# Optimization experiments

Measured on AMD Instinct MI355X. Metric: run time of the kernel, lower is better.

## Reference

```python
import jax, jax.numpy as jnp
import numpy as np

K = 9  # ATSS top-k candidates per GT


def cxcywh_to_xyxy(b):
    cx, cy, w, h = b[..., 0], b[..., 1], b[..., 2], b[..., 3]
    return jnp.stack([cx - 0.5 * w, cy - 0.5 * h, cx + 0.5 * w, cy + 0.5 * h], axis=-1)


def elementwise_iou(a, b):
    # a, b: [..., 4] xyxy, broadcastable
    lt = jnp.maximum(a[..., :2], b[..., :2])
    rb = jnp.minimum(a[..., 2:], b[..., 2:])
    wh = jnp.clip(rb - lt, 0.0)
    inter = wh[..., 0] * wh[..., 1]
    area_a = (a[..., 2] - a[..., 0]) * (a[..., 3] - a[..., 1])
    area_b = (b[..., 2] - b[..., 0]) * (b[..., 3] - b[..., 1])
    return inter / (area_a + area_b - inter)


def setup_inputs() -> dict:
    key = jax.random.key(0)
    k1, k2 = jax.random.split(key)
    pred_boxes = jax.random.uniform(k1, (16, 30000, 4), dtype=jnp.float32)
    gt_boxes = jax.random.uniform(k2, (16, 64, 4), dtype=jnp.float32)
    return {"pred_boxes": pred_boxes, "gt_boxes": gt_boxes}


def reference(pred_boxes, gt_boxes):
    # pred_boxes: [B, N, 4] cxcywh; gt_boxes: [B, G, 4] cxcywh
    G = gt_boxes.shape[1]

    def per_image(pred, gt):
        # center-distance matrix [G, N] (the cdist in the original)
        diff = gt[:, None, :2] - pred[None, :, :2]
        dist = jnp.sqrt(jnp.sum(diff * diff, axis=-1))
        # k smallest distances per GT
        _, k_idx = jax.lax.top_k(-dist, K)          # [G, K]
        k_boxes = pred[k_idx]                        # [G, K, 4]
        gt_xyxy = cxcywh_to_xyxy(gt)                 # [G, 4]
        kb_xyxy = cxcywh_to_xyxy(k_boxes)            # [G, K, 4]
        ious = elementwise_iou(gt_xyxy[:, None, :], kb_xyxy)  # [G, K]
        # adaptive threshold: mean + std (torch.std is unbiased -> ddof=1)
        thr = jnp.mean(ious, axis=1, keepdims=True) + jnp.std(ious, axis=1, ddof=1, keepdims=True)
        cx, cy = k_boxes[..., 0], k_boxes[..., 1]
        inside = ((gt_xyxy[:, None, 0] <= cx) & (cx <= gt_xyxy[:, None, 2]) &
                  (gt_xyxy[:, None, 1] <= cy) & (cy <= gt_xyxy[:, None, 3]))
        mask = (ious >= thr) & inside                # [G, K]
        # padded index representation (original returns ragged lists):
        pred_idx = jnp.where(mask, k_idx, -1)
        gt_idx = jnp.where(mask, jnp.arange(G, dtype=jnp.int64)[:, None], -1)
        return pred_idx, gt_idx, mask, ious

    return jax.vmap(per_image)(pred_boxes, gt_boxes)
```

## Files before the change

kernel.cpp:

```cpp
#include <hip/hip_runtime.h>
#include <stdint.h>

typedef unsigned long long u64;

#define KCAND 9
#define BATCH 16
#define NPRED 30000
#define NGT   64
#define TPB   256
#define UNR   8
#define NT    15
#define INITKEY 0x7F800000FFFFFFFFULL

__device__ __forceinline__ u64 wave_min_u64(u64 v) {
#pragma unroll
    for (int s = 1; s < 64; s <<= 1) {
        u64 o = __shfl_xor(v, s, 64);
        v = o < v ? o : v;
    }
    return v;
}

__global__ __launch_bounds__(256) void compact_xy(
    const float* __restrict__ pred, float2* __restrict__ xy)
{
    int e = blockIdx.x * 256 + threadIdx.x;
    if (e < BATCH * NPRED) {
        float4 p = ((const float4*)pred)[e];
        xy[e] = make_float2(p.x, p.y);
    }
}

template <int S2>
__global__ __launch_bounds__(TPB, 4) void atss_kernel(
    const float2* __restrict__ xy,
    const float*  __restrict__ pred,
    const float*  __restrict__ gt,
    float* __restrict__ out)
{
#pragma clang fp contract(off)
    const int tid  = threadIdx.x;
    const int lane = tid & 63;
    const int wvid = tid >> 6;

    const int b = (blockIdx.x & 7) + 8 * (blockIdx.x >> 9);
    const int g = (blockIdx.x >> 3) & 63;
    const int w = b * NGT + g;

    const float4 gtb = ((const float4*)gt)[w];
    const float gcx = gtb.x, gcy = gtb.y;
    const float2* xyb   = xy + (size_t)b * NPRED * S2;
    const float4* pred4 = (const float4*)pred + (size_t)b * NPRED;

    u64 val = INITKEY;
    float Tf = __uint_as_float(0x7F800000u);

    for (int t = 0; t < NT; ++t) {
        const int i0 = t * (TPB * UNR) + wvid * (64 * UNR) + lane;
        float d2[UNR];
#pragma unroll
        for (int j = 0; j < UNR; ++j) {
            const int i = i0 + j * 64;
            const bool v = i < NPRED;
            float2 p = xyb[(v ? i : 0) * S2];
            float dx = __fsub_rn(gcx, p.x);
            float dy = __fsub_rn(gcy, p.y);
            float d = __fadd_rn(__fmul_rn(dx, dx), __fmul_rn(dy, dy));
            d2[j] = v ? d : __uint_as_float(0x7F800000u);
        }
        float dmin = d2[0];
#pragma unroll
        for (int j = 1; j < UNR; ++j) dmin = fminf(dmin, d2[j]);
        if (__ballot(dmin <= Tf) == 0ULL) continue;

#pragma unroll
        for (int j = 0; j < UNR; ++j) {
            u64 pend = __ballot(d2[j] <= Tf);
            while (pend) {
                const int src = __ffsll(pend) - 1;
                pend &= pend - 1;
                const unsigned kd = __shfl(__float_as_uint(d2[j]), src, 64);
                const unsigned ki = (unsigned)(i0 + j * 64 - lane + src);
                const u64 key = ((u64)kd << 32) | ki;
                u64 Tkey = __shfl(val, 8, 64);
                if (key < Tkey) {
                    const u64 ltm = __ballot(val < key) & 0x1FFULL;
                    const int pos = __popcll(ltm);
                    const u64 sh = __shfl_up(val, 1, 64);
                    if (lane < KCAND) {
                        if (lane == pos)      val = key;
                        else if (lane > pos)  val = sh;
                    }
                    Tkey = __shfl(val, 8, 64);
                    Tf = __uint_as_float((unsigned)(Tkey >> 32));
                    pend &= __ballot(d2[j] <= Tf);
                }
            }
        }
    }

    __shared__ u64 smem[4 * KCAND];
    if (lane < KCAND) smem[wvid * KCAND + lane] = val;
    __syncthreads();

    if (wvid != 0) return;

    u64 key = (lane < 4 * KCAND) ? smem[lane] : ~0ULL;
    u64 fin = 0;
#pragma unroll
    for (int k = 0; k < KCAND; ++k) {
        u64 m = wave_min_u64(key);
        if (lane == k) fin = m;
        if (key == m) key = ~0ULL;
    }

    const bool active = (lane < KCAND);
    const unsigned idx = active ? (unsigned)(fin & 0xffffffffu) : 0u;

    float4 pb = pred4[idx];

    float gx1 = gcx - 0.5f * gtb.z, gy1 = gcy - 0.5f * gtb.w;
    float gx2 = gcx + 0.5f * gtb.z, gy2 = gcy + 0.5f * gtb.w;
    float kx1 = pb.x - 0.5f * pb.z, ky1 = pb.y - 0.5f * pb.w;
    float kx2 = pb.x + 0.5f * pb.z, ky2 = pb.y + 0.5f * pb.w;

    float ltx = fmaxf(gx1, kx1), lty = fmaxf(gy1, ky1);
    float rbx = fminf(gx2, kx2), rby = fminf(gy2, ky2);
    float wvd = fmaxf(rbx - ltx, 0.0f);
    float hvd = fmaxf(rby - lty, 0.0f);
    float inter  = wvd * hvd;
    float area_a = (gx2 - gx1) * (gy2 - gy1);
    float area_b = (kx2 - kx1) * (ky2 - ky1);
    float iou = inter / ((area_a + area_b) - inter);

    float v = active ? iou : 0.0f;
    float s = v;
#pragma unroll
    for (int m = 1; m < 64; m <<= 1) s += __shfl_xor(s, m, 64);
    float mean = s / 9.0f;

    float dev = active ? (iou - mean) : 0.0f;
    float ss = dev * dev;
#pragma unroll
    for (int m = 1; m < 64; m <<= 1) ss += __shfl_xor(ss, m, 64);
    float stdv = sqrtf(ss / 8.0f);
    float thr = mean + stdv;

    bool inside = (gx1 <= pb.x) && (pb.x <= gx2) &&
                  (gy1 <= pb.y) && (pb.y <= gy2);
    bool maskk = (iou >= thr) && inside;

    if (active) {
        const size_t chunk = (size_t)BATCH * NGT * KCAND;
        const size_t o = (size_t)w * KCAND + lane;
        out[0 * chunk + o] = maskk ? (float)idx : -1.0f;
        out[1 * chunk + o] = maskk ? (float)g   : -1.0f;
        out[2 * chunk + o] = maskk ? 1.0f : 0.0f;
        out[3 * chunk + o] = iou;
    }
}

extern "C" void kernel_launch(void* const* d_in, const int* in_sizes, int n_in,
                              void* d_out, int out_size, void* d_ws, size_t ws_size,
                              hipStream_t stream) {
    const float* pred = (const float*)d_in[0];
    const float* gtb  = (const float*)d_in[1];
    float* out = (float*)d_out;

    const size_t need = (size_t)BATCH * NPRED * sizeof(float2);
    if (ws_size >= need) {
        float2* xy = (float2*)d_ws;
        compact_xy<<<(BATCH * NPRED + 255) / 256, 256, 0, stream>>>(pred, xy);
        atss_kernel<1><<<BATCH * NGT, TPB, 0, stream>>>(xy, pred, gtb, out);
    } else {
        atss_kernel<2><<<BATCH * NGT, TPB, 0, stream>>>(
            (const float2*)pred, pred, gtb, out);
    }
}
```

Before: 97.38 us.

## Add threshold pre-pass and padded float4 loads to ATSS top-k scan

Result: faster. 83.43 us (-14.3%).

```diff
diff --git a/kernel.cpp b/kernel.cpp
--- a/kernel.cpp
+++ b/kernel.cpp
@@ -9,8 +9,11 @@
 #define NGT   64
 #define TPB   256
 #define UNR   8
+#define PPT   (TPB * UNR)
 #define NT    15
+#define PSTR  (NT * PPT)
 #define INITKEY 0x7F800000FFFFFFFFULL
+#define FINF  __uint_as_float(0x7F800000u)
 
 __device__ __forceinline__ u64 wave_min_u64(u64 v) {
 #pragma unroll
@@ -25,13 +28,19 @@
     const float* __restrict__ pred, float2* __restrict__ xy)
 {
     int e = blockIdx.x * 256 + threadIdx.x;
-    if (e < BATCH * NPRED) {
-        float4 p = ((const float4*)pred)[e];
-        xy[e] = make_float2(p.x, p.y);
-    }
-}
-
-template <int S2>
+    int b = e / PSTR;
+    int i = e - b * PSTR;
+    float2 v;
+    if (i < NPRED) {
+        float4 p = ((const float4*)pred)[(size_t)b * NPRED + i];
+        v = make_float2(p.x, p.y);
+    } else {
+        v = make_float2(FINF, FINF);
+    }
+    xy[e] = v;
+}
+
+template <bool PADDED>
 __global__ __launch_bounds__(TPB, 4) void atss_kernel(
     const float2* __restrict__ xy,
     const float*  __restrict__ pred,
@@ -49,28 +58,81 @@
 
     const float4 gtb = ((const float4*)gt)[w];
     const float gcx = gtb.x, gcy = gtb.y;
-    const float2* xyb   = xy + (size_t)b * NPRED * S2;
+
+    const int STRIDE = PADDED ? PSTR : (NPRED * 2);
+    const float2* xyb   = xy + (size_t)b * STRIDE;
     const float4* pred4 = (const float4*)pred + (size_t)b * NPRED;
 
+    float lmin = FINF;
+    for (int t = 0; t < NT; ++t) {
+        float d2[UNR];
+        if (PADDED) {
+            const float4* x4 = (const float4*)xyb;
+#pragma unroll
+            for (int k = 0; k < 4; ++k) {
+                float4 q = x4[t * (PPT / 2) + k * TPB + tid];
+                float dx0 = __fsub_rn(gcx, q.x), dy0 = __fsub_rn(gcy, q.y);
+                d2[2 * k]     = __fadd_rn(__fmul_rn(dx0, dx0), __fmul_rn(dy0, dy0));
+                float dx1 = __fsub_rn(gcx, q.z), dy1 = __fsub_rn(gcy, q.w);
+                d2[2 * k + 1] = __fadd_rn(__fmul_rn(dx1, dx1), __fmul_rn(dy1, dy1));
+            }
+        } else {
+#pragma unroll
+            for (int j = 0; j < UNR; ++j) {
+                const int i = t * PPT + j * TPB + tid;
+                const bool v = i < NPRED;
+                float2 p = xyb[(v ? i : 0) * 2];
+                float dx = __fsub_rn(gcx, p.x), dy = __fsub_rn(gcy, p.y);
+                float d = __fadd_rn(__fmul_rn(dx, dx), __fmul_rn(dy, dy));
+                d2[j] = v ? d : FINF;
+            }
+        }
+        float m0 = fminf(d2[0], d2[1]), m1 = fminf(d2[2], d2[3]);
+        float m2 = fminf(d2[4], d2[5]), m3 = fminf(d2[6], d2[7]);
+        lmin = fminf(lmin, fminf(fminf(m0, m1), fminf(m2, m3)));
+    }
+
+    float vv = lmin;
+    float T = FINF;
+#pragma unroll
+    for (int r = 0; r < KCAND; ++r) {
+        float m = vv;
+#pragma unroll
+        for (int s = 1; s < 64; s <<= 1) m = fminf(m, __shfl_xor(m, s, 64));
+        T = m;
+        u64 bm = __ballot(vv == m);
+        if (lane == __ffsll(bm) - 1) vv = FINF;
+    }
+
     u64 val = INITKEY;
-    float Tf = __uint_as_float(0x7F800000u);
+    float Tf = T;
 
     for (int t = 0; t < NT; ++t) {
-        const int i0 = t * (TPB * UNR) + wvid * (64 * UNR) + lane;
         float d2[UNR];
-#pragma unroll
-        for (int j = 0; j < UNR; ++j) {
-            const int i = i0 + j * 64;
-            const bool v = i < NPRED;
-            float2 p = xyb[(v ? i : 0) * S2];
-            float dx = __fsub_rn(gcx, p.x);
-            float dy = __fsub_rn(gcy, p.y);
-            float d = __fadd_rn(__fmul_rn(dx, dx), __fmul_rn(dy, dy));
-            d2[j] = v ? d : __uint_as_float(0x7F800000u);
+        if (PADDED) {
+            const float4* x4 = (const float4*)xyb;
+#pragma unroll
+            for (int k = 0; k < 4; ++k) {
+                float4 q = x4[t * (PPT / 2) + k * TPB + tid];
+                float dx0 = __fsub_rn(gcx, q.x), dy0 = __fsub_rn(gcy, q.y);
+                d2[2 * k]     = __fadd_rn(__fmul_rn(dx0, dx0), __fmul_rn(dy0, dy0));
+                float dx1 = __fsub_rn(gcx, q.z), dy1 = __fsub_rn(gcy, q.w);
+                d2[2 * k + 1] = __fadd_rn(__fmul_rn(dx1, dx1), __fmul_rn(dy1, dy1));
+            }
+        } else {
+#pragma unroll
+            for (int j = 0; j < UNR; ++j) {
+                const int i = t * PPT + j * TPB + tid;
+                const bool v = i < NPRED;
+                float2 p = xyb[(v ? i : 0) * 2];
+                float dx = __fsub_rn(gcx, p.x), dy = __fsub_rn(gcy, p.y);
+                float d = __fadd_rn(__fmul_rn(dx, dx), __fmul_rn(dy, dy));
+                d2[j] = v ? d : FINF;
+            }
         }
-        float dmin = d2[0];
-#pragma unroll
-        for (int j = 1; j < UNR; ++j) dmin = fminf(dmin, d2[j]);
+        float m0 = fminf(d2[0], d2[1]), m1 = fminf(d2[2], d2[3]);
+        float m2 = fminf(d2[4], d2[5]), m3 = fminf(d2[6], d2[7]);
+        float dmin = fminf(fminf(m0, m1), fminf(m2, m3));
         if (__ballot(dmin <= Tf) == 0ULL) continue;
 
 #pragma unroll
@@ -80,7 +142,13 @@
                 const int src = __ffsll(pend) - 1;
                 pend &= pend - 1;
                 const unsigned kd = __shfl(__float_as_uint(d2[j]), src, 64);
-                const unsigned ki = (unsigned)(i0 + j * 64 - lane + src);
+                unsigned ki;
+                if (PADDED) {
+                    const int f = t * (PPT / 2) + (j >> 1) * TPB + (tid - lane) + src;
+                    ki = (unsigned)(2 * f + (j & 1));
+                } else {
+                    ki = (unsigned)(t * PPT + j * TPB + (tid - lane) + src);
+                }
                 const u64 key = ((u64)kd << 32) | ki;
                 u64 Tkey = __shfl(val, 8, 64);
                 if (key < Tkey) {
@@ -92,7 +160,7 @@
                         else if (lane > pos)  val = sh;
                     }
                     Tkey = __shfl(val, 8, 64);
-                    Tf = __uint_as_float((unsigned)(Tkey >> 32));
+                    Tf = fminf(T, __uint_as_float((unsigned)(Tkey >> 32)));
                     pend &= __ballot(d2[j] <= Tf);
                 }
             }
@@ -167,13 +235,13 @@
     const float* gtb  = (const float*)d_in[1];
     float* out = (float*)d_out;
 
-    const size_t need = (size_t)BATCH * NPRED * sizeof(float2);
+    const size_t need = (size_t)BATCH * PSTR * sizeof(float2);
     if (ws_size >= need) {
         float2* xy = (float2*)d_ws;
-        compact_xy<<<(BATCH * NPRED + 255) / 256, 256, 0, stream>>>(pred, xy);
-        atss_kernel<1><<<BATCH * NGT, TPB, 0, stream>>>(xy, pred, gtb, out);
+        compact_xy<<<BATCH * PSTR / 256, 256, 0, stream>>>(pred, xy);
+        atss_kernel<true><<<BATCH * NGT, TPB, 0, stream>>>(xy, pred, gtb, out);
     } else {
-        atss_kernel<2><<<BATCH * NGT, TPB, 0, stream>>>(
+        atss_kernel<false><<<BATCH * NGT, TPB, 0, stream>>>(
             (const float2*)pred, pred, gtb, out);
     }
 }
```

## Process two GTs per block with two-pass threshold prefilter, drop xy compaction

Applied to the files above, without the earlier changes.

Measured after the change: 85.43 us. 12.3% less time.

```diff
diff --git a/kernel.cpp b/kernel.cpp
--- a/kernel.cpp
+++ b/kernel.cpp
@@ -9,8 +9,12 @@
 #define NGT   64
 #define TPB   256
 #define UNR   8
-#define NT    15
+#define PPT   (TPB * UNR)
+#define NFULL 14
+#define TAILB (NFULL * PPT)
+#define TSLOT 6
 #define INITKEY 0x7F800000FFFFFFFFULL
+#define FINF  __uint_as_float(0x7F800000u)
 
 __device__ __forceinline__ u64 wave_min_u64(u64 v) {
 #pragma unroll
@@ -21,91 +25,157 @@
     return v;
 }
 
-__global__ __launch_bounds__(256) void compact_xy(
-    const float* __restrict__ pred, float2* __restrict__ xy)
-{
-    int e = blockIdx.x * 256 + threadIdx.x;
-    if (e < BATCH * NPRED) {
-        float4 p = ((const float4*)pred)[e];
-        xy[e] = make_float2(p.x, p.y);
-    }
-}
-
-template <int S2>
-__global__ __launch_bounds__(TPB, 4) void atss_kernel(
-    const float2* __restrict__ xy,
-    const float*  __restrict__ pred,
-    const float*  __restrict__ gt,
+__global__ __launch_bounds__(TPB, 2) void atss_pair(
+    const float* __restrict__ pred,
+    const float* __restrict__ gt,
     float* __restrict__ out)
 {
 #pragma clang fp contract(off)
-    const int tid  = threadIdx.x;
-    const int lane = tid & 63;
-    const int wvid = tid >> 6;
-
-    const int b = (blockIdx.x & 7) + 8 * (blockIdx.x >> 9);
-    const int g = (blockIdx.x >> 3) & 63;
-    const int w = b * NGT + g;
-
-    const float4 gtb = ((const float4*)gt)[w];
-    const float gcx = gtb.x, gcy = gtb.y;
-    const float2* xyb   = xy + (size_t)b * NPRED * S2;
-    const float4* pred4 = (const float4*)pred + (size_t)b * NPRED;
-
-    u64 val = INITKEY;
-    float Tf = __uint_as_float(0x7F800000u);
-
-    for (int t = 0; t < NT; ++t) {
-        const int i0 = t * (TPB * UNR) + wvid * (64 * UNR) + lane;
-        float d2[UNR];
+    const int tid   = threadIdx.x;
+    const int lane  = tid & 63;
+    const int wvid  = tid >> 6;
+    const int wbase = wvid << 6;
+
+    const int bi = blockIdx.x;
+    const int b  = (bi & 7) + 8 * (bi >> 8);
+    const int gp = (bi >> 3) & 31;
+    const int g0 = 2 * gp;
+
+    const float4* gt4 = (const float4*)gt;
+    const float4 gA = gt4[b * NGT + g0];
+    const float4 gB = gt4[b * NGT + g0 + 1];
+    const float aX = gA.x, aY = gA.y;
+    const float bX = gB.x, bY = gB.y;
+    const float4* pb = (const float4*)pred + (size_t)b * NPRED;
+
+    float lmA = FINF, lmB = FINF;
+    for (int t = 0; t < NFULL; ++t) {
+        const int base = t * PPT + tid;
 #pragma unroll
         for (int j = 0; j < UNR; ++j) {
-            const int i = i0 + j * 64;
+            float4 q = pb[base + j * TPB];
+            float dxA = __fsub_rn(aX, q.x), dyA = __fsub_rn(aY, q.y);
+            float dA = __fadd_rn(__fmul_rn(dxA, dxA), __fmul_rn(dyA, dyA));
+            float dxB = __fsub_rn(bX, q.x), dyB = __fsub_rn(bY, q.y);
+            float dB = __fadd_rn(__fmul_rn(dxB, dxB), __fmul_rn(dyB, dyB));
+            lmA = fminf(lmA, dA);
+            lmB = fminf(lmB, dB);
+        }
+    }
+#pragma unroll
+    for (int j = 0; j < TSLOT; ++j) {
+        const int i = TAILB + j * TPB + tid;
+        const bool v = i < NPRED;
+        float4 q = pb[v ? i : 0];
+        float dxA = __fsub_rn(aX, q.x), dyA = __fsub_rn(aY, q.y);
+        float dA = __fadd_rn(__fmul_rn(dxA, dxA), __fmul_rn(dyA, dyA));
+        float dxB = __fsub_rn(bX, q.x), dyB = __fsub_rn(bY, q.y);
+        float dB = __fadd_rn(__fmul_rn(dxB, dxB), __fmul_rn(dyB, dyB));
+        lmA = fminf(lmA, v ? dA : FINF);
+        lmB = fminf(lmB, v ? dB : FINF);
+    }
+
+    float vA = lmA, vB = lmB;
+    float TA = FINF, TB = FINF;
+#pragma unroll
+    for (int r = 0; r < KCAND; ++r) {
+        float mA = vA, mB = vB;
+#pragma unroll
+        for (int s = 1; s < 64; s <<= 1) {
+            mA = fminf(mA, __shfl_xor(mA, s, 64));
+            mB = fminf(mB, __shfl_xor(mB, s, 64));
+        }
+        TA = mA; TB = mB;
+        u64 eA = __ballot(vA == mA);
+        if (lane == __ffsll(eA) - 1) vA = FINF;
+        u64 eB = __ballot(vB == mB);
+        if (lane == __ffsll(eB) - 1) vB = FINF;
+    }
+
+    u64 valA = INITKEY, valB = INITKEY;
+    float TfA = TA, TfB = TB;
+
+#define INSERT(DARR, VAL, TF, TBOUND, KI_BASE)                                 \
+    {                                                                          \
+        u64 pend = __ballot((DARR) <= (TF));                                   \
+        while (pend) {                                                         \
+            const int src = __ffsll(pend) - 1;                                 \
+            pend &= pend - 1;                                                  \
+            const unsigned kd = __shfl(__float_as_uint(DARR), src, 64);        \
+            const unsigned ki = (unsigned)((KI_BASE) + src);                   \
+            const u64 key = ((u64)kd << 32) | ki;                              \
+            u64 Tkey = __shfl((VAL), 8, 64);                                   \
+            if (key < Tkey) {                                                  \
+                const u64 ltm = __ballot((VAL) < key) & 0x1FFULL;              \
+                const int pos = __popcll(ltm);                                 \
+                const u64 sh = __shfl_up((VAL), 1, 64);                        \
+                if (lane < KCAND) {                                            \
+                    if (lane == pos)      (VAL) = key;                         \
+                    else if (lane > pos)  (VAL) = sh;                          \
+                }                                                              \
+                Tkey = __shfl((VAL), 8, 64);                                   \
+                (TF) = fminf((TBOUND), __uint_as_float((unsigned)(Tkey >> 32)));\
+                pend &= __ballot((DARR) <= (TF));                              \
+            }                                                                  \
+        }                                                                      \
+    }
+
+    for (int t = 0; t < NFULL; ++t) {
+        const int base = t * PPT + tid;
+        float dA[UNR], dB[UNR];
+#pragma unroll
+        for (int j = 0; j < UNR; ++j) {
+            float4 q = pb[base + j * TPB];
+            float dxA = __fsub_rn(aX, q.x), dyA = __fsub_rn(aY, q.y);
+            dA[j] = __fadd_rn(__fmul_rn(dxA, dxA), __fmul_rn(dyA, dyA));
+            float dxB = __fsub_rn(bX, q.x), dyB = __fsub_rn(bY, q.y);
+            dB[j] = __fadd_rn(__fmul_rn(dxB, dxB), __fmul_rn(dyB, dyB));
+        }
+        float mA0 = fminf(fminf(dA[0], dA[1]), fminf(dA[2], dA[3]));
+        float mA1 = fminf(fminf(dA[4], dA[5]), fminf(dA[6], dA[7]));
+        float mB0 = fminf(fminf(dB[0], dB[1]), fminf(dB[2], dB[3]));
+        float mB1 = fminf(fminf(dB[4], dB[5]), fminf(dB[6], dB[7]));
+        float dmA = fminf(mA0, mA1), dmB = fminf(mB0, mB1);
+        if ((__ballot(dmA <= TfA) | __ballot(dmB <= TfB)) == 0ULL) continue;
+
+#pragma unroll
+        for (int j = 0; j < UNR; ++j) {
+            INSERT(dA[j], valA, TfA, TA, t * PPT + j * TPB + wbase);
+            INSERT(dB[j], valB, TfB, TB, t * PPT + j * TPB + wbase);
+        }
+    }
+    {
+        float dA[TSLOT], dB[TSLOT];
+#pragma unroll
+        for (int j = 0; j < TSLOT; ++j) {
+            const int i = TAILB + j * TPB + tid;
             const bool v = i < NPRED;
-            float2 p = xyb[(v ? i : 0) * S2];
-            float dx = __fsub_rn(gcx, p.x);
-            float dy = __fsub_rn(gcy, p.y);
-            float d = __fadd_rn(__fmul_rn(dx, dx), __fmul_rn(dy, dy));
-            d2[j] = v ? d : __uint_as_float(0x7F800000u);
-        }
-        float dmin = d2[0];
-#pragma unroll
-        for (int j = 1; j < UNR; ++j) dmin = fminf(dmin, d2[j]);
-        if (__ballot(dmin <= Tf) == 0ULL) continue;
-
-#pragma unroll
-        for (int j = 0; j < UNR; ++j) {
-            u64 pend = __ballot(d2[j] <= Tf);
-            while (pend) {
-                const int src = __ffsll(pend) - 1;
-                pend &= pend - 1;
-                const unsigned kd = __shfl(__float_as_uint(d2[j]), src, 64);
-                const unsigned ki = (unsigned)(i0 + j * 64 - lane + src);
-                const u64 key = ((u64)kd << 32) | ki;
-                u64 Tkey = __shfl(val, 8, 64);
-                if (key < Tkey) {
-                    const u64 ltm = __ballot(val < key) & 0x1FFULL;
-                    const int pos = __popcll(ltm);
-                    const u64 sh = __shfl_up(val, 1, 64);
-                    if (lane < KCAND) {
-                        if (lane == pos)      val = key;
-                        else if (lane > pos)  val = sh;
-                    }
-                    Tkey = __shfl(val, 8, 64);
-                    Tf = __uint_as_float((unsigned)(Tkey >> 32));
-                    pend &= __ballot(d2[j] <= Tf);
-                }
-            }
-        }
-    }
-
-    __shared__ u64 smem[4 * KCAND];
-    if (lane < KCAND) smem[wvid * KCAND + lane] = val;
+            float4 q = pb[v ? i : 0];
+            float dxA = __fsub_rn(aX, q.x), dyA = __fsub_rn(aY, q.y);
+            float dTA = __fadd_rn(__fmul_rn(dxA, dxA), __fmul_rn(dyA, dyA));
+            float dxB = __fsub_rn(bX, q.x), dyB = __fsub_rn(bY, q.y);
+            float dTB = __fadd_rn(__fmul_rn(dxB, dxB), __fmul_rn(dyB, dyB));
+            dA[j] = v ? dTA : FINF;
+            dB[j] = v ? dTB : FINF;
+        }
+#pragma unroll
+        for (int j = 0; j < TSLOT; ++j) {
+            INSERT(dA[j], valA, TfA, TA, TAILB + j * TPB + wbase);
+            INSERT(dB[j], valB, TfB, TB, TAILB + j * TPB + wbase);
+        }
+    }
+#undef INSERT
+
+    __shared__ u64 smem[2][4 * KCAND];
+    if (lane < KCAND) {
+        smem[0][wvid * KCAND + lane] = valA;
+        smem[1][wvid * KCAND + lane] = valB;
+    }
     __syncthreads();
 
-    if (wvid != 0) return;
-
-    u64 key = (lane < 4 * KCAND) ? smem[lane] : ~0ULL;
+    if (wvid >= 2) return;
+
+    u64 key = (lane < 4 * KCAND) ? smem[wvid][lane] : ~0ULL;
     u64 fin = 0;
 #pragma unroll
     for (int k = 0; k < KCAND; ++k) {
@@ -114,15 +184,20 @@
         if (key == m) key = ~0ULL;
     }
 
+    const int g = g0 + wvid;
+    const int w = b * NGT + g;
+    const float4 gq = wvid ? gB : gA;
+    const float gcx = gq.x, gcy = gq.y;
+
     const bool active = (lane < KCAND);
     const unsigned idx = active ? (unsigned)(fin & 0xffffffffu) : 0u;
 
-    float4 pb = pred4[idx];
-
-    float gx1 = gcx - 0.5f * gtb.z, gy1 = gcy - 0.5f * gtb.w;
-    float gx2 = gcx + 0.5f * gtb.z, gy2 = gcy + 0.5f * gtb.w;
-    float kx1 = pb.x - 0.5f * pb.z, ky1 = pb.y - 0.5f * pb.w;
-    float kx2 = pb.x + 0.5f * pb.z, ky2 = pb.y + 0.5f * pb.w;
+    float4 pbx = pb[idx];
+
+    float gx1 = gcx - 0.5f * gq.z, gy1 = gcy - 0.5f * gq.w;
+    float gx2 = gcx + 0.5f * gq.z, gy2 = gcy + 0.5f * gq.w;
+    float kx1 = pbx.x - 0.5f * pbx.z, ky1 = pbx.y - 0.5f * pbx.w;
+    float kx2 = pbx.x + 0.5f * pbx.z, ky2 = pbx.y + 0.5f * pbx.w;
 
     float ltx = fmaxf(gx1, kx1), lty = fmaxf(gy1, ky1);
     float rbx = fminf(gx2, kx2), rby = fminf(gy2, ky2);
@@ -146,8 +221,8 @@
     float stdv = sqrtf(ss / 8.0f);
     float thr = mean + stdv;
 
-    bool inside = (gx1 <= pb.x) && (pb.x <= gx2) &&
-                  (gy1 <= pb.y) && (pb.y <= gy2);
+    bool inside = (gx1 <= pbx.x) && (pbx.x <= gx2) &&
+                  (gy1 <= pbx.y) && (pbx.y <= gy2);
     bool maskk = (iou >= thr) && inside;
 
     if (active) {
@@ -166,14 +241,7 @@
     const float* pred = (const float*)d_in[0];
     const float* gtb  = (const float*)d_in[1];
     float* out = (float*)d_out;
-
-    const size_t need = (size_t)BATCH * NPRED * sizeof(float2);
-    if (ws_size >= need) {
-        float2* xy = (float2*)d_ws;
-        compact_xy<<<(BATCH * NPRED + 255) / 256, 256, 0, stream>>>(pred, xy);
-        atss_kernel<1><<<BATCH * NGT, TPB, 0, stream>>>(xy, pred, gtb, out);
-    } else {
-        atss_kernel<2><<<BATCH * NGT, TPB, 0, stream>>>(
-            (const float2*)pred, pred, gtb, out);
-    }
+    (void)d_ws; (void)ws_size;
+
+    atss_pair<<<BATCH * (NGT / 2), TPB, 0, stream>>>(pred, gtb, out);
 }
```

## Replace brute-force top-k scan with uniform-grid binning and ring search

Applied to the files above, without the earlier changes.

Result: slower. 117.7 us (+20.9%).

```diff
diff --git a/kernel.cpp b/kernel.cpp
--- a/kernel.cpp
+++ b/kernel.cpp
@@ -2,15 +2,17 @@
 #include <stdint.h>
 
 typedef unsigned long long u64;
+typedef unsigned int u32;
 
 #define KCAND 9
 #define BATCH 16
 #define NPRED 30000
 #define NGT   64
-#define TPB   256
-#define UNR   8
-#define NT    15
-#define INITKEY 0x7F800000FFFFFFFFULL
+#define NCELL 1024
+#define CDIM  32
+#define CELLW (1.0f / 32.0f)
+#define SENT  (~0ULL)
+#define FINF  __uint_as_float(0x7F800000u)
 
 __device__ __forceinline__ u64 wave_min_u64(u64 v) {
 #pragma unroll
@@ -20,109 +22,58 @@
     }
     return v;
 }
-
-__global__ __launch_bounds__(256) void compact_xy(
-    const float* __restrict__ pred, float2* __restrict__ xy)
-{
-    int e = blockIdx.x * 256 + threadIdx.x;
-    if (e < BATCH * NPRED) {
-        float4 p = ((const float4*)pred)[e];
-        xy[e] = make_float2(p.x, p.y);
-    }
-}
-
-template <int S2>
-__global__ __launch_bounds__(TPB, 4) void atss_kernel(
-    const float2* __restrict__ xy,
-    const float*  __restrict__ pred,
-    const float*  __restrict__ gt,
-    float* __restrict__ out)
-{
+__device__ __forceinline__ float wave_min_f(float v) {
+#pragma unroll
+    for (int s = 1; s < 64; s <<= 1) v = fminf(v, __shfl_xor(v, s, 64));
+    return v;
+}
+__device__ __forceinline__ u32 wave_iscan_u32(u32 v, int lane) {
+#pragma unroll
+    for (int s = 1; s < 64; s <<= 1) {
+        u32 t = __shfl_up(v, s, 64);
+        if (lane >= s) v += t;
+    }
+    return v;
+}
+
+#define DIST(GX, GY, PX, PY, D)                                              \
+    { float _dx = __fsub_rn(GX, PX), _dy = __fsub_rn(GY, PY);                \
+      D = __fadd_rn(__fmul_rn(_dx, _dx), __fmul_rn(_dy, _dy)); }
+
+__device__ __forceinline__ u64 merge9(u64 val, u64 bk, int lane) {
+    u64 a = (lane < KCAND) ? val : SENT;
+    u64 nv = SENT;
+#pragma unroll
+    for (int r = 0; r < KCAND; ++r) {
+        u64 ml = a < bk ? a : bk;
+        u64 m = wave_min_u64(ml);
+        if (lane == r) nv = m;
+        if (a == m) a = SENT;
+        else if (bk == m) bk = SENT;
+    }
+    return nv;
+}
+
+__device__ __forceinline__ int cell_of(float x, float y) {
+    int cx = (int)(x * 32.0f); cx = cx < 0 ? 0 : (cx > 31 ? 31 : cx);
+    int cy = (int)(y * 32.0f); cy = cy < 0 ? 0 : (cy > 31 ? 31 : cy);
+    return (cy << 5) | cx;
+}
+
+__device__ void atss_epilogue(u64 fin, int b, int g, const float4* p4,
+                              float4 gq, float* __restrict__ out, int lane) {
 #pragma clang fp contract(off)
-    const int tid  = threadIdx.x;
-    const int lane = tid & 63;
-    const int wvid = tid >> 6;
-
-    const int b = (blockIdx.x & 7) + 8 * (blockIdx.x >> 9);
-    const int g = (blockIdx.x >> 3) & 63;
     const int w = b * NGT + g;
-
-    const float4 gtb = ((const float4*)gt)[w];
-    const float gcx = gtb.x, gcy = gtb.y;
-    const float2* xyb   = xy + (size_t)b * NPRED * S2;
-    const float4* pred4 = (const float4*)pred + (size_t)b * NPRED;
-
-    u64 val = INITKEY;
-    float Tf = __uint_as_float(0x7F800000u);
-
-    for (int t = 0; t < NT; ++t) {
-        const int i0 = t * (TPB * UNR) + wvid * (64 * UNR) + lane;
-        float d2[UNR];
-#pragma unroll
-        for (int j = 0; j < UNR; ++j) {
-            const int i = i0 + j * 64;
-            const bool v = i < NPRED;
-            float2 p = xyb[(v ? i : 0) * S2];
-            float dx = __fsub_rn(gcx, p.x);
-            float dy = __fsub_rn(gcy, p.y);
-            float d = __fadd_rn(__fmul_rn(dx, dx), __fmul_rn(dy, dy));
-            d2[j] = v ? d : __uint_as_float(0x7F800000u);
-        }
-        float dmin = d2[0];
-#pragma unroll
-        for (int j = 1; j < UNR; ++j) dmin = fminf(dmin, d2[j]);
-        if (__ballot(dmin <= Tf) == 0ULL) continue;
-
-#pragma unroll
-        for (int j = 0; j < UNR; ++j) {
-            u64 pend = __ballot(d2[j] <= Tf);
-            while (pend) {
-                const int src = __ffsll(pend) - 1;
-                pend &= pend - 1;
-                const unsigned kd = __shfl(__float_as_uint(d2[j]), src, 64);
-                const unsigned ki = (unsigned)(i0 + j * 64 - lane + src);
-                const u64 key = ((u64)kd << 32) | ki;
-                u64 Tkey = __shfl(val, 8, 64);
-                if (key < Tkey) {
-                    const u64 ltm = __ballot(val < key) & 0x1FFULL;
-                    const int pos = __popcll(ltm);
-                    const u64 sh = __shfl_up(val, 1, 64);
-                    if (lane < KCAND) {
-                        if (lane == pos)      val = key;
-                        else if (lane > pos)  val = sh;
-                    }
-                    Tkey = __shfl(val, 8, 64);
-                    Tf = __uint_as_float((unsigned)(Tkey >> 32));
-                    pend &= __ballot(d2[j] <= Tf);
-                }
-            }
-        }
-    }
-
-    __shared__ u64 smem[4 * KCAND];
-    if (lane < KCAND) smem[wvid * KCAND + lane] = val;
-    __syncthreads();
-
-    if (wvid != 0) return;
-
-    u64 key = (lane < 4 * KCAND) ? smem[lane] : ~0ULL;
-    u64 fin = 0;
-#pragma unroll
-    for (int k = 0; k < KCAND; ++k) {
-        u64 m = wave_min_u64(key);
-        if (lane == k) fin = m;
-        if (key == m) key = ~0ULL;
-    }
-
+    const float gcx = gq.x, gcy = gq.y;
     const bool active = (lane < KCAND);
     const unsigned idx = active ? (unsigned)(fin & 0xffffffffu) : 0u;
 
-    float4 pb = pred4[idx];
-
-    float gx1 = gcx - 0.5f * gtb.z, gy1 = gcy - 0.5f * gtb.w;
-    float gx2 = gcx + 0.5f * gtb.z, gy2 = gcy + 0.5f * gtb.w;
-    float kx1 = pb.x - 0.5f * pb.z, ky1 = pb.y - 0.5f * pb.w;
-    float kx2 = pb.x + 0.5f * pb.z, ky2 = pb.y + 0.5f * pb.w;
+    float4 pbx = p4[idx];
+
+    float gx1 = gcx - 0.5f * gq.z, gy1 = gcy - 0.5f * gq.w;
+    float gx2 = gcx + 0.5f * gq.z, gy2 = gcy + 0.5f * gq.w;
+    float kx1 = pbx.x - 0.5f * pbx.z, ky1 = pbx.y - 0.5f * pbx.w;
+    float kx2 = pbx.x + 0.5f * pbx.z, ky2 = pbx.y + 0.5f * pbx.w;
 
     float ltx = fmaxf(gx1, kx1), lty = fmaxf(gy1, ky1);
     float rbx = fminf(gx2, kx2), rby = fminf(gy2, ky2);
@@ -146,8 +97,8 @@
     float stdv = sqrtf(ss / 8.0f);
     float thr = mean + stdv;
 
-    bool inside = (gx1 <= pb.x) && (pb.x <= gx2) &&
-                  (gy1 <= pb.y) && (pb.y <= gy2);
+    bool inside = (gx1 <= pbx.x) && (pbx.x <= gx2) &&
+                  (gy1 <= pbx.y) && (pbx.y <= gy2);
     bool maskk = (iou >= thr) && inside;
 
     if (active) {
@@ -160,6 +111,167 @@
     }
 }
 
+__global__ __launch_bounds__(512) void bin_scatter(
+    const float* __restrict__ pred, float4* __restrict__ scat,
+    u32* __restrict__ mstart, u32* __restrict__ mcount)
+{
+    const int b    = blockIdx.x;
+    const int tid  = threadIdx.x;
+    const int lane = tid & 63;
+    const int wv   = tid >> 6;
+
+    const float4* p4 = (const float4*)pred + (size_t)b * NPRED;
+
+    __shared__ u32 hist[NCELL];
+    __shared__ u32 cur[NCELL];
+    __shared__ u32 wtot[8];
+
+    for (int c = tid; c < NCELL; c += 512) hist[c] = 0;
+    __syncthreads();
+
+    for (int i = tid; i < NPRED; i += 512) {
+        float4 p = p4[i];
+        atomicAdd(&hist[cell_of(p.x, p.y)], 1u);
+    }
+    __syncthreads();
+
+    const int c0 = (wv << 7) + lane, c1 = c0 + 64;
+    u32 a0 = hist[c0], a1 = hist[c1];
+    u32 s0 = wave_iscan_u32(a0, lane);
+    u32 t0 = __shfl(s0, 63, 64);
+    u32 s1 = wave_iscan_u32(a1, lane) + t0;
+    if (lane == 63) wtot[wv] = s1;
+    __syncthreads();
+    u32 off = 0;
+    for (int k = 0; k < wv; ++k) off += wtot[k];
+    const u32 st0 = off + s0 - a0, st1 = off + s1 - a1;
+    cur[c0] = st0;  cur[c1] = st1;
+    mstart[b * NCELL + c0] = st0;  mstart[b * NCELL + c1] = st1;
+    mcount[b * NCELL + c0] = a0;   mcount[b * NCELL + c1] = a1;
+    __syncthreads();
+
+    for (int i = tid; i < NPRED; i += 512) {
+        float4 p = p4[i];
+        u32 slot = atomicAdd(&cur[cell_of(p.x, p.y)], 1u);
+        scat[(size_t)b * NPRED + slot] =
+            make_float4(p.x, p.y, __uint_as_float((u32)i), 0.0f);
+    }
+}
+
+__global__ __launch_bounds__(64) void atss_search(
+    const float4* __restrict__ scat, const u32* __restrict__ mstart,
+    const u32* __restrict__ mcount,  const float* __restrict__ pred,
+    const float* __restrict__ gt,    float* __restrict__ out)
+{
+#pragma clang fp contract(off)
+    const int bi   = blockIdx.x;
+    const int lane = threadIdx.x;
+    const int b    = bi & 15;
+    const int g    = bi >> 4;
+
+    const float4 gq = ((const float4*)gt)[b * NGT + g];
+    const float gx = gq.x, gy = gq.y;
+    int cx = (int)(gx * 32.0f); cx = cx < 0 ? 0 : (cx > 31 ? 31 : cx);
+    int cy = (int)(gy * 32.0f); cy = cy < 0 ? 0 : (cy > 31 ? 31 : cy);
+
+    const float4* sb  = scat + (size_t)b * NPRED;
+    const u32*    msb = mstart + b * NCELL;
+    const u32*    mcb = mcount + b * NCELL;
+
+    u64 val = SENT;
+
+#define PCELL(CX, CY)                                                        \
+    { const int _cc = ((CY) << 5) | (CX);                                    \
+      const u32 _st = msb[_cc], _cn = mcb[_cc];                              \
+      for (u32 _off = 0; _off < _cn; _off += 64) {                           \
+          u64 bk = SENT;                                                     \
+          const u32 _ii = _off + (u32)lane;                                  \
+          if (_ii < _cn) {                                                   \
+              float4 q = sb[_st + _ii];                                      \
+              float dd; DIST(gx, gy, q.x, q.y, dd);                          \
+              bk = ((u64)__float_as_uint(dd) << 32)                         \
+                   | (u64)(u32)__float_as_uint(q.z);                         \
+          }                                                                  \
+          u64 bmin = wave_min_u64(bk);                                       \
+          u64 k8s  = __shfl(val, 8, 64);                                     \
+          if (bmin < k8s) val = merge9(val, bk, lane);                       \
+      } }
+
+    for (int m = 0;; ++m) {
+        if (m == 0) {
+            PCELL(cx, cy)
+        } else {
+            const int x0 = cx - m, x1 = cx + m, y0 = cy - m, y1 = cy + m;
+            const int xa = x0 < 0 ? 0 : x0, xb = x1 > 31 ? 31 : x1;
+            if (y0 >= 0) { for (int x = xa; x <= xb; ++x) PCELL(x, y0) }
+            if (y1 <= 31){ for (int x = xa; x <= xb; ++x) PCELL(x, y1) }
+            const int ya = (y0 + 1) < 0 ? 0 : (y0 + 1);
+            const int yb = (y1 - 1) > 31 ? 31 : (y1 - 1);
+            if (x0 >= 0) { for (int y = ya; y <= yb; ++y) PCELL(x0, y) }
+            if (x1 <= 31){ for (int y = ya; y <= yb; ++y) PCELL(x1, y) }
+        }
+        const u64 k8 = __shfl(val, 8, 64);
+        if (k8 != SENT) {
+            const float d9f = __uint_as_float((u32)(k8 >> 32));
+            float bd = (float)m * CELLW;
+            const float bd2 = bd * bd * (1.0f - 1e-5f);
+            if (d9f < bd2) break;
+        }
+        if (m >= 31) break;
+    }
+#undef PCELL
+
+    atss_epilogue(val, b, g, (const float4*)pred + (size_t)b * NPRED,
+                  gq, out, lane);
+}
+
+__global__ __launch_bounds__(64) void atss_fullscan(
+    const float* __restrict__ pred, const float* __restrict__ gt,
+    float* __restrict__ out)
+{
+#pragma clang fp contract(off)
+    const int bi   = blockIdx.x;
+    const int lane = threadIdx.x;
+    const int b    = bi & 15;
+    const int g    = bi >> 4;
+
+    const float4 gq = ((const float4*)gt)[b * NGT + g];
+    const float gx = gq.x, gy = gq.y;
+    const float4* p4 = (const float4*)pred + (size_t)b * NPRED;
+
+    float lm = FINF;
+    for (int i = lane; i < NPRED; i += 64) {
+        float4 q = p4[i];
+        float d; DIST(gx, gy, q.x, q.y, d);
+        lm = fminf(lm, d);
+    }
+    float vv = lm, T = FINF;
+#pragma unroll
+    for (int r = 0; r < KCAND; ++r) {
+        float m = wave_min_f(vv);
+        T = m;
+        u64 e = __ballot(vv == m);
+        if (lane == __ffsll(e) - 1) vv = FINF;
+    }
+
+    u64 val = SENT;
+    for (int i0 = 0; i0 < NPRED; i0 += 64) {
+        const int i = i0 + lane;
+        u64 bk = SENT;
+        if (i < NPRED) {
+            float4 q = p4[i];
+            float d; DIST(gx, gy, q.x, q.y, d);
+            if (d <= T) bk = ((u64)__float_as_uint(d) << 32) | (u32)i;
+        }
+        if (__ballot(bk != SENT)) {
+            u64 bmin = wave_min_u64(bk);
+            u64 k8s  = __shfl(val, 8, 64);
+            if (bmin < k8s) val = merge9(val, bk, lane);
+        }
+    }
+    atss_epilogue(val, b, g, p4, gq, out, lane);
+}
+
 extern "C" void kernel_launch(void* const* d_in, const int* in_sizes, int n_in,
                               void* d_out, int out_size, void* d_ws, size_t ws_size,
                               hipStream_t stream) {
@@ -167,13 +279,16 @@
     const float* gtb  = (const float*)d_in[1];
     float* out = (float*)d_out;
 
-    const size_t need = (size_t)BATCH * NPRED * sizeof(float2);
-    if (ws_size >= need) {
-        float2* xy = (float2*)d_ws;
-        compact_xy<<<(BATCH * NPRED + 255) / 256, 256, 0, stream>>>(pred, xy);
-        atss_kernel<1><<<BATCH * NGT, TPB, 0, stream>>>(xy, pred, gtb, out);
+    const size_t scat_bytes = (size_t)BATCH * NPRED * sizeof(float4);
+    const size_t meta_bytes = (size_t)2 * BATCH * NCELL * sizeof(u32);
+    if (ws_size >= scat_bytes + meta_bytes) {
+        float4* scat  = (float4*)d_ws;
+        u32* mstart   = (u32*)((char*)d_ws + scat_bytes);
+        u32* mcount   = mstart + BATCH * NCELL;
+        bin_scatter<<<BATCH, 512, 0, stream>>>(pred, scat, mstart, mcount);
+        atss_search<<<BATCH * NGT, 64, 0, stream>>>(
+            scat, mstart, mcount, pred, gtb, out);
     } else {
-        atss_kernel<2><<<BATCH * NGT, TPB, 0, stream>>>(
-            (const float2*)pred, pred, gtb, out);
-    }
-}
+        atss_fullscan<<<BATCH * NGT, 64, 0, stream>>>(pred, gtb, out);
+    }
+}
```
